# Optimization experiments

Measured on AMD Instinct MI355X. Metric: run time of the kernel, lower is better.

## Reference

```python
import jax, jax.numpy as jnp
import numpy as np

D = 128      # embedding dim
T = 8        # message passing rounds (config.training.T)
NV = 4000    # n_vars
NL = 2 * NV  # n_literals
NC = 16000   # n_clauses


def setup_inputs() -> dict:
    key = jax.random.key(0)
    ks = jax.random.split(key, 12)
    s = np.float32(1.0 / np.sqrt(D))
    return {
        "L_state": jax.random.normal(ks[0], (1, NL, D), jnp.float32),
        "C_state": jax.random.normal(ks[1], (1, NC, D), jnp.float32),
        "hidden_L": jnp.zeros((1, NL, D), jnp.float32),
        "hidden_C": jnp.zeros((1, NC, D), jnp.float32),
        # 0/1 literal-clause incidence, ~40 clauses per literal
        "M": (jax.random.uniform(ks[2], (NL, NC)) < 0.0025).astype(jnp.float32),
        "n_vars": NV,
        "W_lc": jax.random.normal(ks[3], (D, D), jnp.float32) * s,
        "b_lc": jnp.zeros((D,), jnp.float32),
        "W_cl": jax.random.normal(ks[4], (D, D), jnp.float32) * s,
        "b_cl": jnp.zeros((D,), jnp.float32),
        "Wih_C": jax.random.normal(ks[5], (4 * D, D), jnp.float32) * s,
        "Whh_C": jax.random.normal(ks[6], (4 * D, D), jnp.float32) * s,
        "bih_C": jnp.zeros((4 * D,), jnp.float32),
        "bhh_C": jnp.zeros((4 * D,), jnp.float32),
        "Wih_L": jax.random.normal(ks[7], (4 * D, 2 * D), jnp.float32) * s,
        "Whh_L": jax.random.normal(ks[8], (4 * D, D), jnp.float32) * s,
        "bih_L": jnp.zeros((4 * D,), jnp.float32),
        "bhh_L": jnp.zeros((4 * D,), jnp.float32),
    }


def lstm_cell(x, h, c, Wih, Whh, bih, bhh):
    # torch nn.LSTM gate order: i, f, g, o
    gates = x @ Wih.T + bih + h @ Whh.T + bhh
    i, f, g, o = jnp.split(gates, 4, axis=-1)
    c_new = jax.nn.sigmoid(f) * c + jax.nn.sigmoid(i) * jnp.tanh(g)
    h_new = jax.nn.sigmoid(o) * jnp.tanh(c_new)
    return h_new, c_new


def reference(L_state, C_state, hidden_L, hidden_C, M, n_vars,
              W_lc, b_lc, W_cl, b_cl,
              Wih_C, Whh_C, bih_C, bhh_C,
              Wih_L, Whh_L, bih_L, bhh_L):
    # Replicates torch flip() as written: slices dim 0 (size 1), so this is
    # effectively identity for n_vars >= 1 (first slice is empty, second is x).
    def flip(x):
        return jnp.concatenate([x[n_vars:2 * n_vars], x[0:n_vars]], axis=0)

    def step(carry, _):
        L, hL, hC = carry
        LC_pre = L @ W_lc.T + b_lc                        # (1, NL, D)
        LC_msgs = jnp.einsum('lc,sld->scd', M, LC_pre)    # M^T @ pre: (1, NC, D)
        Cs, hC = lstm_cell(LC_msgs, hC, hC, Wih_C, Whh_C, bih_C, bhh_C)
        CL_pre = Cs @ W_cl.T + b_cl                       # (1, NC, D)
        CL_msgs = jnp.einsum('lc,scd->sld', M, CL_pre)    # M @ pre: (1, NL, D)
        inp = jnp.concatenate([CL_msgs, flip(L)], axis=2) # (1, NL, 2D)
        L, hL = lstm_cell(inp, hL, hL, Wih_L, Whh_L, bih_L, bhh_L)
        return (L, hL, hC), None

    (L_final, _, _), _ = jax.lax.scan(step, (L_state, hidden_L, hidden_C), None, length=T)
    return L_final
```

## Files before the change

kernel.cpp:

```cpp
#include <hip/hip_runtime.h>

#define DD   128
#define NL   8000
#define NC   16000
#define TSTEPS 8
#define NBF  2
#define ROWW 96
#define COLW 64

#define OS   33
#define SPLITS8 (32 * OS)
#define SPLIT   (SPLITS8 * 8)
#define LSTR 17
#define LSPL (48 * LSTR * 8)
#define L2S  33
#define L2SPL (48 * L2S * 8)

typedef __attribute__((ext_vector_type(8))) short  short8;
typedef __attribute__((ext_vector_type(8))) _Float16 half8;
typedef __attribute__((ext_vector_type(4))) float  f32x4;

__device__ __forceinline__ float frcp(float x) { return __builtin_amdgcn_rcpf(x); }
__device__ __forceinline__ float sigm(float x) { return frcp(1.f + __expf(-x)); }
__device__ __forceinline__ float tanh_(float x) {
  float e = __expf(2.f * x);
  return 1.f - 2.f * frcp(e + 1.f);
}
__device__ __forceinline__ void add4(float4& a, const float4 b) {
  a.x += b.x; a.y += b.y; a.z += b.z; a.w += b.w;
}
__device__ __forceinline__ unsigned short bfround(float v) {
  unsigned u = __float_as_uint(v);
  return (unsigned short)((u + 0x7FFF + ((u >> 16) & 1)) >> 16);
}
__device__ __forceinline__ float bf2f(unsigned short b) {
  return __uint_as_float(((unsigned)b) << 16);
}
__device__ __forceinline__ void splitf16(float v, unsigned short& h, unsigned short& l) {
  _Float16 hh = (_Float16)v;
  float r = v - (float)hh;
  _Float16 ll = (_Float16)r;
  h = __builtin_bit_cast(unsigned short, hh);
  l = __builtin_bit_cast(unsigned short, ll);
}
__device__ __forceinline__ int4 packi4(const unsigned short* p) {
  return make_int4(p[0] | ((int)p[1] << 16), p[2] | ((int)p[3] << 16),
                   p[4] | ((int)p[5] << 16), p[6] | ((int)p[7] << 16));
}

__device__ __forceinline__ void store_oct3(unsigned short* A, int oct, int m,
                                           float4 a, float4 b) {
  float f[8] = {a.x, a.y, a.z, a.w, b.x, b.y, b.z, b.w};
  unsigned short h[8], md[8], lo[8];
  #pragma unroll
  for (int j = 0; j < 8; ++j) {
    h[j] = bfround(f[j]);
    float r1 = f[j] - bf2f(h[j]);
    md[j] = bfround(r1);
    float r2 = r1 - bf2f(md[j]);
    lo[j] = bfround(r2);
  }
  int base = (oct * OS + m) * 8;
  *(int4*)(A + base)             = packi4(h);
  *(int4*)(A + SPLIT + base)     = packi4(md);
  *(int4*)(A + 2 * SPLIT + base) = packi4(lo);
}

__device__ __forceinline__ void store_oct2g(unsigned short* A, int strideS8, int plane,
                                            int oct, int m, float4 a, float4 b) {
  float f[8] = {a.x, a.y, a.z, a.w, b.x, b.y, b.z, b.w};
  unsigned short h[8], lo[8];
  #pragma unroll
  for (int j = 0; j < 8; ++j) splitf16(f[j], h[j], lo[j]);
  int base = (oct * strideS8 + m) * 8;
  *(int4*)(A + base)         = packi4(h);
  *(int4*)(A + plane + base) = packi4(lo);
}

__device__ __forceinline__ void store_half3L(unsigned short* A, int oct, int half, int m,
                                             float4 a) {
  float f[4] = {a.x, a.y, a.z, a.w};
  unsigned short h[4], md[4], lo[4];
  #pragma unroll
  for (int j = 0; j < 4; ++j) {
    h[j] = bfround(f[j]);
    float r1 = f[j] - bf2f(h[j]);
    md[j] = bfround(r1);
    float r2 = r1 - bf2f(md[j]);
    lo[j] = bfround(r2);
  }
  int base = (oct * LSTR + m) * 8 + half * 4;
  *(int2*)(A + base)            = make_int2(h[0]  | ((int)h[1]  << 16), h[2]  | ((int)h[3]  << 16));
  *(int2*)(A + LSPL + base)     = make_int2(md[0] | ((int)md[1] << 16), md[2] | ((int)md[3] << 16));
  *(int2*)(A + 2 * LSPL + base) = make_int2(lo[0] | ((int)lo[1] << 16), lo[2] | ((int)lo[3] << 16));
}

#define MFMA6(ACC, AH, AM, AL, BH, BM, BL)                                   \
  ACC = __builtin_amdgcn_mfma_f32_16x16x32_bf16(AH, BH, ACC, 0, 0, 0);       \
  ACC = __builtin_amdgcn_mfma_f32_16x16x32_bf16(AH, BM, ACC, 0, 0, 0);       \
  ACC = __builtin_amdgcn_mfma_f32_16x16x32_bf16(AM, BH, ACC, 0, 0, 0);       \
  ACC = __builtin_amdgcn_mfma_f32_16x16x32_bf16(AH, BL, ACC, 0, 0, 0);       \
  ACC = __builtin_amdgcn_mfma_f32_16x16x32_bf16(AL, BH, ACC, 0, 0, 0);       \
  ACC = __builtin_amdgcn_mfma_f32_16x16x32_bf16(AM, BM, ACC, 0, 0, 0);

#define MFMA4(ACC, AH, AL, BH, BL)                                           \
  ACC = __builtin_amdgcn_mfma_f32_16x16x32_f16(AH, BH, ACC, 0, 0, 0);        \
  ACC = __builtin_amdgcn_mfma_f32_16x16x32_f16(AH, BL, ACC, 0, 0, 0);        \
  ACC = __builtin_amdgcn_mfma_f32_16x16x32_f16(AL, BH, ACC, 0, 0, 0);        \
  ACC = __builtin_amdgcn_mfma_f32_16x16x32_f16(AL, BL, ACC, 0, 0, 0);


__global__ __launch_bounds__(256) void init_states(
    float4* __restrict__ Lbuf, const float4* __restrict__ L0,
    float4* __restrict__ hL, const float4* __restrict__ hL0,
    float4* __restrict__ hC, const float4* __restrict__ hC0) {
  int i = blockIdx.x * 256 + threadIdx.x, stride = gridDim.x * 256;
  for (int j = i; j < NL * DD / 4; j += stride) { Lbuf[j] = L0[j]; hL[j] = hL0[j]; }
  for (int j = i; j < NC * DD / 4; j += stride) hC[j] = hC0[j];
}

__global__ __launch_bounds__(256) void scan_M(const float4* __restrict__ M4,
                                              int* __restrict__ csr, int* __restrict__ csc,
                                              int* __restrict__ rcnt, int* __restrict__ ccnt) {
  const int total = (NL * NC) / 4;
  int stride = gridDim.x * blockDim.x;
  for (int i = blockIdx.x * blockDim.x + threadIdx.x; i < total; i += stride) {
    float4 v = M4[i];
    if (v.x == 0.f && v.y == 0.f && v.z == 0.f && v.w == 0.f) continue;
    int base = i * 4;
    int l = base / NC;
    int c0 = base - l * NC;
    float vv[4] = {v.x, v.y, v.z, v.w};
    #pragma unroll
    for (int e = 0; e < 4; ++e) {
      if (vv[e] != 0.f) {
        int c = c0 + e;
        int rp = atomicAdd(&rcnt[l], 1);
        if (rp < ROWW) csr[l * ROWW + rp] = c;
        int cp = atomicAdd(&ccnt[c], 1);
        if (cp < COLW) csc[c * COLW + cp] = l;
      }
    }
  }
}

__device__ __forceinline__ void split_store_bf3(float w, int idx, unsigned short* hi,
                                                unsigned short* md, unsigned short* lo) {
  unsigned short h = bfround(w);
  float r1 = w - bf2f(h);
  unsigned short m = bfround(r1);
  float r2 = r1 - bf2f(m);
  hi[idx] = h; md[idx] = m; lo[idx] = bfround(r2);
}

__global__ __launch_bounds__(256) void build_packC(
    const float* __restrict__ WihC, const float* __restrict__ Wlc, const float* __restrict__ WhhC,
    unsigned short* __restrict__ pkhi, unsigned short* __restrict__ pkmd, unsigned short* __restrict__ pklo,
    unsigned short* __restrict__ qkhi, unsigned short* __restrict__ qklo) {
  int i = blockIdx.x * 256 + threadIdx.x;
  int k = i >> 9, n = i & 511;
  float w;
  if (k < 128) {
    float s = 0.f;
    for (int d = 0; d < 128; ++d) s += WihC[n * 128 + d] * Wlc[d * 128 + k];
    w = s;
  } else {
    w = WhhC[n * 128 + (k - 128)];
  }
  int idx = ((k >> 3) * 512 + n) * 8 + (k & 7);
  split_store_bf3(w, idx, pkhi, pkmd, pklo);
  splitf16(w, qkhi[idx], qklo[idx]);
}

__global__ __launch_bounds__(256) void build_packL(
    const float* __restrict__ WihL, const float* __restrict__ Wcl, const float* __restrict__ WhhL,
    unsigned short* __restrict__ pkhi, unsigned short* __restrict__ pkmd, unsigned short* __restrict__ pklo,
    unsigned short* __restrict__ qkhi, unsigned short* __restrict__ qklo) {
  int i = blockIdx.x * 256 + threadIdx.x;
  int k = i >> 9, n = i & 511;
  float w;
  if (k < 128) {
    float s = 0.f;
    for (int d = 0; d < 128; ++d) s += WihL[n * 256 + d] * Wcl[d * 128 + k];
    w = s;
  } else if (k < 256) {
    w = WihL[n * 256 + k];
  } else {
    w = WhhL[n * 128 + (k - 256)];
  }
  int idx = ((k >> 3) * 512 + n) * 8 + (k & 7);
  split_store_bf3(w, idx, pkhi, pkmd, pklo);
  splitf16(w, qkhi[idx], qklo[idx]);
}

__global__ __launch_bounds__(256) void build_bias(
    const float* __restrict__ bihC, const float* __restrict__ bhhC,
    const float* __restrict__ WihC, const float* __restrict__ blc,
    const float* __restrict__ bihL, const float* __restrict__ bhhL,
    const float* __restrict__ WihL, const float* __restrict__ bcl,
    float* __restrict__ bsumC, float* __restrict__ bvecC,
    float* __restrict__ bsumL, float* __restrict__ bvecL) {
  int i = blockIdx.x * 256 + threadIdx.x;
  if (i < 512) {
    bsumC[i] = bihC[i] + bhhC[i];
    float s = 0.f;
    for (int d = 0; d < 128; ++d) s += WihC[i * 128 + d] * blc[d];
    bvecC[i] = s;
  } else if (i < 1024) {
    int n = i - 512;
    bsumL[n] = bihL[n] + bhhL[n];
    float s = 0.f;
    for (int d = 0; d < 128; ++d) s += WihL[n * 256 + d] * bcl[d];
    bvecL[n] = s;
  }
}

__device__ __forceinline__ void clause_epilogue(
    const f32x4 acc[2][4], const float* bsum, const float* bvec, const int* ccnt,
    float* hC, float* Cs, int rowBase, int quad, int cw) {
  float bs_[4], bv_[4];
  #pragma unroll
  for (int g = 0; g < 4; ++g) { bs_[g] = bsum[g * 128 + cw]; bv_[g] = bvec[g * 128 + cw]; }
  #pragma unroll
  for (int mt = 0; mt < 2; ++mt) {
    #pragma unroll
    for (int reg = 0; reg < 4; ++reg) {
      int row = rowBase + mt * 16 + quad * 4 + reg;
      float deg = (float)ccnt[row];
      float co = hC[(size_t)row * DD + cw];
      float iv = acc[mt][0][reg] + bs_[0] + deg * bv_[0];
      float fv = acc[mt][1][reg] + bs_[1] + deg * bv_[1];
      float gv = acc[mt][2][reg] + bs_[2] + deg * bv_[2];
      float ov = acc[mt][3][reg] + bs_[3] + deg * bv_[3];
      float cn = sigm(fv) * co + sigm(iv) * tanh_(gv);
      hC[(size_t)row * DD + cw] = cn;
      Cs[(size_t)row * DD + cw] = sigm(ov) * tanh_(cn);
    }
  }
}

__device__ __forceinline__ void literal_epilogue2(
    const f32x4 acc[2][4], const float* bsum, const float* bvec, const int* rcnt,
    float* hL, float* Lbuf, int rowBase, int quad, int cw) {
  float bs_[4], bv_[4];
  #pragma unroll
  for (int g = 0; g < 4; ++g) { bs_[g] = bsum[g * 128 + cw]; bv_[g] = bvec[g * 128 + cw]; }
  #pragma unroll
  for (int mt = 0; mt < 2; ++mt) {
    #pragma unroll
    for (int reg = 0; reg < 4; ++reg) {
      int row = rowBase + mt * 16 + quad * 4 + reg;
      float deg = (float)rcnt[row];
      float co = hL[(size_t)row * DD + cw];
      float iv = acc[mt][0][reg] + bs_[0] + deg * bv_[0];
      float fv = acc[mt][1][reg] + bs_[1] + deg * bv_[1];
      float gv = acc[mt][2][reg] + bs_[2] + deg * bv_[2];
      float ov = acc[mt][3][reg] + bs_[3] + deg * bv_[3];
      float cn = sigm(fv) * co + sigm(iv) * tanh_(gv);
      hL[(size_t)row * DD + cw] = cn;
      Lbuf[(size_t)row * DD + cw] = sigm(ov) * tanh_(cn);
    }
  }
}


template <int NOCT, bool STAGE_H>
__global__ __launch_bounds__(512, 4) void clause_bf3(
    const float* __restrict__ Lbuf, const int* __restrict__ csc, const int* __restrict__ ccnt,
    const unsigned short* __restrict__ pkhi, const unsigned short* __restrict__ pkmd,
    const unsigned short* __restrict__ pklo,
    const float* __restrict__ bsum, const float* __restrict__ bvec,
    float* __restrict__ hC, float* __restrict__ Cs) {
  __shared__ unsigned short A[3 * SPLIT];
  __shared__ int IDX[32 * COLW];
  const int t = threadIdx.x;
  const int rowBase = blockIdx.x * 32;

  ((int4*)IDX)[t] = ((const int4*)(csc + rowBase * COLW))[t];
  __syncthreads();

  {
    const int r = t >> 4, sub = t & 15;
    const int c = rowBase + r;
    int cnt = ccnt[c]; if (cnt > COLW) cnt = COLW;
    const int* lst = IDX + r * COLW;
    float4 a0 = make_float4(0, 0, 0, 0), a1 = a0;
    int j = 0;
    for (; j + 8 <= cnt; j += 8) {
      float4 p0[8], p1[8];
      #pragma unroll
      for (int u = 0; u < 8; ++u) {
        const float4* s4 = (const float4*)(Lbuf + (size_t)lst[j + u] * DD) + sub * 2;
        p0[u] = s4[0]; p1[u] = s4[1];
      }
      #pragma unroll
      for (int u = 0; u < 8; ++u) { add4(a0, p0[u]); add4(a1, p1[u]); }
    }
    for (; j < cnt; ++j) {
      const float4* s4 = (const float4*)(Lbuf + (size_t)lst[j] * DD) + sub * 2;
      add4(a0, s4[0]); add4(a1, s4[1]);
    }
    store_oct3(A, sub, r, a0, a1);
    if constexpr (STAGE_H) {
      const float4* h4 = (const float4*)(hC + (size_t)c * DD) + sub * 2;
      store_oct3(A, 16 + sub, r, h4[0], h4[1]);
    }
  }
  __syncthreads();

  const int w = t >> 6, l = t & 63;
  const int quad = l >> 4, lane16 = l & 15;
  const int cw = w * 16 + lane16;
  f32x4 acc[2][4];
  #pragma unroll
  for (int mt = 0; mt < 2; ++mt)
    #pragma unroll
    for (int g = 0; g < 4; ++g) acc[mt][g] = (f32x4){0.f, 0.f, 0.f, 0.f};

  const short8* As = (const short8*)A;
  const short8* Bh = (const short8*)pkhi;
  const short8* Bm = (const short8*)pkmd;
  const short8* Bl = (const short8*)pklo;

  __builtin_amdgcn_s_setprio(1);
  #pragma unroll
  for (int s = 0; s < NOCT / 4; ++s) {
    int ao = (s * 4 + quad) * OS + lane16;
    short8 a0h = As[ao],                a1h = As[ao + 16];
    short8 a0m = As[SPLITS8 + ao],      a1m = As[SPLITS8 + ao + 16];
    short8 a0l = As[2 * SPLITS8 + ao],  a1l = As[2 * SPLITS8 + ao + 16];
    int bo = (s * 4 + quad) * 512 + cw;
    #pragma unroll
    for (int g = 0; g < 4; ++g) {
      short8 bh = Bh[bo + g * 128];
      short8 bm = Bm[bo + g * 128];
      short8 bl = Bl[bo + g * 128];
      MFMA6(acc[0][g], a0h, a0m, a0l, bh, bm, bl);
      MFMA6(acc[1][g], a1h, a1m, a1l, bh, bm, bl);
    }
  }
  __builtin_amdgcn_s_setprio(0);
  clause_epilogue(acc, bsum, bvec, ccnt, hC, Cs, rowBase, quad, cw);
}

template <int NOCT, bool STAGE_H>
__global__ __launch_bounds__(512, 4) void literal_bf3(
    const float* __restrict__ Cs, const int* __restrict__ csr, const int* __restrict__ rcnt,
    const unsigned short* __restrict__ pkhi, const unsigned short* __restrict__ pkmd,
    const unsigned short* __restrict__ pklo,
    const float* __restrict__ bsum, const float* __restrict__ bvec,
    float* __restrict__ hL, float* __restrict__ Lbuf) {
  __shared__ unsigned short A[3 * LSPL];
  __shared__ int IDX[16 * ROWW];
  const int t = threadIdx.x;
  const int rowBase = blockIdx.x * 16;

  if (t < 384) ((int4*)IDX)[t] = ((const int4*)(csr + rowBase * ROWW))[t];
  __syncthreads();

  {
    const int r = t >> 5, cg2 = t & 31;
    const int lr = rowBase + r;
    int cnt = rcnt[lr]; if (cnt > ROWW) cnt = ROWW;
    const int* lst = IDX + r * ROWW;
    float4 a0 = make_float4(0, 0, 0, 0);
    int j = 0;
    for (; j + 8 <= cnt; j += 8) {
      float4 p[8];
      #pragma unroll
      for (int u = 0; u < 8; ++u)
        p[u] = ((const float4*)(Cs + (size_t)lst[j + u] * DD))[cg2];
      #pragma unroll
      for (int u = 0; u < 8; ++u) add4(a0, p[u]);
    }
    for (; j < cnt; ++j)
      add4(a0, ((const float4*)(Cs + (size_t)lst[j] * DD))[cg2]);
    store_half3L(A, cg2 >> 1, cg2 & 1, r, a0);
    store_half3L(A, 16 + (cg2 >> 1), cg2 & 1, r,
                 ((const float4*)(Lbuf + (size_t)lr * DD))[cg2]);
    if constexpr (STAGE_H)
      store_half3L(A, 32 + (cg2 >> 1), cg2 & 1, r,
                   ((const float4*)(hL + (size_t)lr * DD))[cg2]);
  }
  __syncthreads();

  const int w = t >> 6, l = t & 63;
  const int quad = l >> 4, lane16 = l & 15;
  const int cw = w * 16 + lane16;
  f32x4 acc[4];
  #pragma unroll
  for (int g = 0; g < 4; ++g) acc[g] = (f32x4){0.f, 0.f, 0.f, 0.f};

  const short8* As = (const short8*)A;
  const short8* Bh = (const short8*)pkhi;
  const short8* Bm = (const short8*)pkmd;
  const short8* Bl = (const short8*)pklo;

  __builtin_amdgcn_s_setprio(1);
  #pragma unroll
  for (int s = 0; s < NOCT / 4; ++s) {
    int ao = (s * 4 + quad) * LSTR + lane16;
    short8 ah = As[ao];
    short8 am = As[LSPL / 8 + ao];
    short8 al = As[2 * (LSPL / 8) + ao];
    int bo = (s * 4 + quad) * 512 + cw;
    #pragma unroll
    for (int g = 0; g < 4; ++g) {
      short8 bh = Bh[bo + g * 128];
      short8 bm = Bm[bo + g * 128];
      short8 bl = Bl[bo + g * 128];
      MFMA6(acc[g], ah, am, al, bh, bm, bl);
    }
  }
  __builtin_amdgcn_s_setprio(0);

  float bs_[4], bv_[4];
  #pragma unroll
  for (int g = 0; g < 4; ++g) { bs_[g] = bsum[g * 128 + cw]; bv_[g] = bvec[g * 128 + cw]; }
  #pragma unroll
  for (int reg = 0; reg < 4; ++reg) {
    int row = rowBase + quad * 4 + reg;
    float deg = (float)rcnt[row];
    float co = hL[(size_t)row * DD + cw];
    float iv = acc[0][reg] + bs_[0] + deg * bv_[0];
    float fv = acc[1][reg] + bs_[1] + deg * bv_[1];
    float gv = acc[2][reg] + bs_[2] + deg * bv_[2];
    float ov = acc[3][reg] + bs_[3] + deg * bv_[3];
    float cn = sigm(fv) * co + sigm(iv) * tanh_(gv);
    hL[(size_t)row * DD + cw] = cn;
    Lbuf[(size_t)row * DD + cw] = sigm(ov) * tanh_(cn);
  }
}


__global__ __launch_bounds__(512, 4) void clause_f2(
    const float* __restrict__ Lbuf, const int* __restrict__ csc, const int* __restrict__ ccnt,
    const unsigned short* __restrict__ qkhi, const unsigned short* __restrict__ qklo,
    const float* __restrict__ bsum, const float* __restrict__ bvec,
    float* __restrict__ hC, float* __restrict__ Cs) {
  __shared__ unsigned short A[2 * SPLIT];
  __shared__ int IDX[32 * COLW];
  const int t = threadIdx.x;
  const int rowBase = blockIdx.x * 32;

  ((int4*)IDX)[t] = ((const int4*)(csc + rowBase * COLW))[t];
  __syncthreads();

  {
    const int r = t >> 4, sub = t & 15;
    const int c = rowBase + r;
    int cnt = ccnt[c]; if (cnt > COLW) cnt = COLW;
    const int* lst = IDX + r * COLW;
    float4 a0 = make_float4(0, 0, 0, 0), a1 = a0;
    int j = 0;
    for (; j + 8 <= cnt; j += 8) {
      float4 p0[8], p1[8];
      #pragma unroll
      for (int u = 0; u < 8; ++u) {
        const float4* s4 = (const float4*)(Lbuf + (size_t)lst[j + u] * DD) + sub * 2;
        p0[u] = s4[0]; p1[u] = s4[1];
      }
      #pragma unroll
      for (int u = 0; u < 8; ++u) { add4(a0, p0[u]); add4(a1, p1[u]); }
    }
    for (; j < cnt; ++j) {
      const float4* s4 = (const float4*)(Lbuf + (size_t)lst[j] * DD) + sub * 2;
      add4(a0, s4[0]); add4(a1, s4[1]);
    }
    store_oct2g(A, OS, SPLIT, sub, r, a0, a1);
    const float4* h4 = (const float4*)(hC + (size_t)c * DD) + sub * 2;
    store_oct2g(A, OS, SPLIT, 16 + sub, r, h4[0], h4[1]);
  }
  __syncthreads();

  const int w = t >> 6, l = t & 63;
  const int quad = l >> 4, lane16 = l & 15;
  const int cw = w * 16 + lane16;
  f32x4 acc[2][4];
  #pragma unroll
  for (int mt = 0; mt < 2; ++mt)
    #pragma unroll
    for (int g = 0; g < 4; ++g) acc[mt][g] = (f32x4){0.f, 0.f, 0.f, 0.f};

  const half8* As = (const half8*)A;
  const half8* Bh = (const half8*)qkhi;
  const half8* Bl = (const half8*)qklo;

  __builtin_amdgcn_s_setprio(1);
  #pragma unroll
  for (int s = 0; s < 8; ++s) {
    int ao = (s * 4 + quad) * OS + lane16;
    half8 a0h = As[ao],           a1h = As[ao + 16];
    half8 a0l = As[SPLITS8 + ao], a1l = As[SPLITS8 + ao + 16];
    int bo = (s * 4 + quad) * 512 + cw;
    #pragma unroll
    for (int g = 0; g < 4; ++g) {
      half8 bh = Bh[bo + g * 128];
      half8 bl = Bl[bo + g * 128];
      MFMA4(acc[0][g], a0h, a0l, bh, bl);
      MFMA4(acc[1][g], a1h, a1l, bh, bl);
    }
  }
  __builtin_amdgcn_s_setprio(0);
  clause_epilogue(acc, bsum, bvec, ccnt, hC, Cs, rowBase, quad, cw);
}

__global__ __launch_bounds__(512, 4) void literal_f2(
    const float* __restrict__ Cs, const int* __restrict__ csr, const int* __restrict__ rcnt,
    const unsigned short* __restrict__ qkhi, const unsigned short* __restrict__ qklo,
    const float* __restrict__ bsum, const float* __restrict__ bvec,
    float* __restrict__ hL, float* __restrict__ Lbuf) {
  __shared__ unsigned short A[2 * L2SPL];
  __shared__ int IDX[32 * ROWW];
  const int t = threadIdx.x;
  const int rowBase = blockIdx.x * 32;

  ((int4*)IDX)[t] = ((const int4*)(csr + rowBase * ROWW))[t];
  if (t < 256) ((int4*)IDX)[t + 512] = ((const int4*)(csr + rowBase * ROWW))[t + 512];
  __syncthreads();

  {
    const int r = t >> 4, sub = t & 15;
    const int lr = rowBase + r;
    int cnt = rcnt[lr]; if (cnt > ROWW) cnt = ROWW;
    const int* lst = IDX + r * ROWW;
    float4 a0 = make_float4(0, 0, 0, 0), a1 = a0;
    int j = 0;
    for (; j + 8 <= cnt; j += 8) {
      float4 p0[8], p1[8];
      #pragma unroll
      for (int u = 0; u < 8; ++u) {
        const float4* s4 = (const float4*)(Cs + (size_t)lst[j + u] * DD) + sub * 2;
        p0[u] = s4[0]; p1[u] = s4[1];
      }
      #pragma unroll
      for (int u = 0; u < 8; ++u) { add4(a0, p0[u]); add4(a1, p1[u]); }
    }
    for (; j < cnt; ++j) {
      const float4* s4 = (const float4*)(Cs + (size_t)lst[j] * DD) + sub * 2;
      add4(a0, s4[0]); add4(a1, s4[1]);
    }
    store_oct2g(A, L2S, L2SPL, sub, r, a0, a1);
    const float4* l4 = (const float4*)(Lbuf + (size_t)lr * DD) + sub * 2;
    store_oct2g(A, L2S, L2SPL, 16 + sub, r, l4[0], l4[1]);
    const float4* h4 = (const float4*)(hL + (size_t)lr * DD) + sub * 2;
    store_oct2g(A, L2S, L2SPL, 32 + sub, r, h4[0], h4[1]);
  }
  __syncthreads();

  const int w = t >> 6, l = t & 63;
  const int quad = l >> 4, lane16 = l & 15;
  const int cw = w * 16 + lane16;
  f32x4 acc[2][4];
  #pragma unroll
  for (int mt = 0; mt < 2; ++mt)
    #pragma unroll
    for (int g = 0; g < 4; ++g) acc[mt][g] = (f32x4){0.f, 0.f, 0.f, 0.f};

  const half8* As = (const half8*)A;
  const half8* Bh = (const half8*)qkhi;
  const half8* Bl = (const half8*)qklo;

  __builtin_amdgcn_s_setprio(1);
  #pragma unroll
  for (int s = 0; s < 12; ++s) {
    int ao = (s * 4 + quad) * L2S + lane16;
    half8 a0h = As[ao],             a1h = As[ao + 16];
    half8 a0l = As[L2SPL / 8 + ao], a1l = As[L2SPL / 8 + ao + 16];
    int bo = (s * 4 + quad) * 512 + cw;
    #pragma unroll
    for (int g = 0; g < 4; ++g) {
      half8 bh = Bh[bo + g * 128];
      half8 bl = Bl[bo + g * 128];
      MFMA4(acc[0][g], a0h, a0l, bh, bl);
      MFMA4(acc[1][g], a1h, a1l, bh, bl);
    }
  }
  __builtin_amdgcn_s_setprio(0);
  literal_epilogue2(acc, bsum, bvec, rcnt, hL, Lbuf, rowBase, quad, cw);
}


extern "C" void kernel_launch(void* const* d_in, const int* in_sizes, int n_in,
                              void* d_out, int out_size, void* d_ws, size_t ws_size,
                              hipStream_t stream) {
  const float* L0   = (const float*)d_in[0];
  const float* hL0  = (const float*)d_in[2];
  const float* hC0  = (const float*)d_in[3];
  const float* M    = (const float*)d_in[4];
  const float* Wlc  = (const float*)d_in[6];
  const float* blc  = (const float*)d_in[7];
  const float* Wcl  = (const float*)d_in[8];
  const float* bcl  = (const float*)d_in[9];
  const float* WihC = (const float*)d_in[10];
  const float* WhhC = (const float*)d_in[11];
  const float* bihC = (const float*)d_in[12];
  const float* bhhC = (const float*)d_in[13];
  const float* WihL = (const float*)d_in[14];
  const float* WhhL = (const float*)d_in[15];
  const float* bihL = (const float*)d_in[16];
  const float* bhhL = (const float*)d_in[17];

  float* ws    = (float*)d_ws;
  float* hL    = ws;
  float* hC    = hL + NL * DD;
  float* Cs    = hC + NC * DD;
  float* bsumC = Cs + NC * DD;
  float* bvecC = bsumC + 512;
  float* bsumL = bvecC + 512;
  float* bvecL = bsumL + 512;
  unsigned short* pkChi = (unsigned short*)(bvecL + 512);
  unsigned short* pkCmd = pkChi + 256 * 512;
  unsigned short* pkClo = pkCmd + 256 * 512;
  unsigned short* pkLhi = pkClo + 256 * 512;
  unsigned short* pkLmd = pkLhi + 384 * 512;
  unsigned short* pkLlo = pkLmd + 384 * 512;
  unsigned short* qkChi = pkLlo + 384 * 512;
  unsigned short* qkClo = qkChi + 256 * 512;
  unsigned short* qkLhi = qkClo + 256 * 512;
  unsigned short* qkLlo = qkLhi + 384 * 512;
  int* csr  = (int*)(qkLlo + 384 * 512);
  int* csc  = csr + NL * ROWW;
  int* rcnt = csc + NC * COLW;
  int* ccnt = rcnt + NL;
  float* Lbuf = (float*)d_out;

  hipMemsetAsync(rcnt, 0, (NL + NC) * sizeof(int), stream);

  init_states<<<1024, 256, 0, stream>>>((float4*)Lbuf, (const float4*)L0,
                                        (float4*)hL, (const float4*)hL0,
                                        (float4*)hC, (const float4*)hC0);

  scan_M<<<4096, 256, 0, stream>>>((const float4*)M, csr, csc, rcnt, ccnt);

  build_packC<<<(256 * 512) / 256, 256, 0, stream>>>(WihC, Wlc, WhhC,
                                                     pkChi, pkCmd, pkClo, qkChi, qkClo);
  build_packL<<<(384 * 512) / 256, 256, 0, stream>>>(WihL, Wcl, WhhL,
                                                     pkLhi, pkLmd, pkLlo, qkLhi, qkLlo);
  build_bias<<<4, 256, 0, stream>>>(bihC, bhhC, WihC, blc, bihL, bhhL, WihL, bcl,
                                    bsumC, bvecC, bsumL, bvecL);

  clause_bf3<16, false><<<NC / 32, 512, 0, stream>>>(Lbuf, csc, ccnt, pkChi, pkCmd, pkClo,
                                                     bsumC, bvecC, hC, Cs);
  literal_bf3<32, false><<<NL / 16, 512, 0, stream>>>(Cs, csr, rcnt, pkLhi, pkLmd, pkLlo,
                                                      bsumL, bvecL, hL, Lbuf);
  for (int t = 1; t < NBF; ++t) {
    clause_bf3<32, true><<<NC / 32, 512, 0, stream>>>(Lbuf, csc, ccnt, pkChi, pkCmd, pkClo,
                                                      bsumC, bvecC, hC, Cs);
    literal_bf3<48, true><<<NL / 16, 512, 0, stream>>>(Cs, csr, rcnt, pkLhi, pkLmd, pkLlo,
                                                       bsumL, bvecL, hL, Lbuf);
  }
  for (int t = NBF; t < TSTEPS; ++t) {
    clause_f2<<<NC / 32, 512, 0, stream>>>(Lbuf, csc, ccnt, qkChi, qkClo,
                                           bsumC, bvecC, hC, Cs);
    literal_f2<<<NL / 32, 512, 0, stream>>>(Cs, csr, rcnt, qkLhi, qkLlo,
                                            bsumL, bvecL, hL, Lbuf);
  }
}
```

Baseline: 1.280 ms.

## Fuse all stages into one persistent cooperative kernel with grid syncs

Replaces the roughly twenty separate launches (memset, init, CSR/CSC scan, weight packing, bias, and the per-step clause and literal kernels) with a single cooperative kernel of 256 blocks. The stages are separated by grid-wide syncs, and each block loops over tiles using a union of the shared-memory layouts. The aim is to remove per-launch overhead and the inter-kernel gaps. The cost is that 256 blocks of 512 threads may give lower occupancy than the earlier larger grids, tiles split unevenly across blocks (500 clause tiles over 256 blocks), and the shared union is sized by its largest member for every stage.

```diff
diff --git a/kernel.cpp b/kernel.cpp
--- a/kernel.cpp
+++ b/kernel.cpp
@@ -1,4 +1,7 @@
 #include <hip/hip_runtime.h>
+#include <hip/hip_cooperative_groups.h>
+
+namespace cg = cooperative_groups;
 
 #define DD   128
 #define NL   8000
@@ -7,6 +10,7 @@
 #define NBF  2
 #define ROWW 96
 #define COLW 64
+#define GRID 256
 
 #define OS   33
 #define SPLITS8 (32 * OS)
@@ -95,6 +99,15 @@
   *(int2*)(A + 2 * LSPL + base) = make_int2(lo[0] | ((int)lo[1] << 16), lo[2] | ((int)lo[3] << 16));
 }
 
+__device__ __forceinline__ void split_store_bf3(float w, int idx, unsigned short* hi,
+                                                unsigned short* md, unsigned short* lo) {
+  unsigned short h = bfround(w);
+  float r1 = w - bf2f(h);
+  unsigned short m = bfround(r1);
+  float r2 = r1 - bf2f(m);
+  hi[idx] = h; md[idx] = m; lo[idx] = bfround(r2);
+}
+
 #define MFMA6(ACC, AH, AM, AL, BH, BM, BL)                                   \
   ACC = __builtin_amdgcn_mfma_f32_16x16x32_bf16(AH, BH, ACC, 0, 0, 0);       \
   ACC = __builtin_amdgcn_mfma_f32_16x16x32_bf16(AH, BM, ACC, 0, 0, 0);       \
@@ -109,111 +122,12 @@
   ACC = __builtin_amdgcn_mfma_f32_16x16x32_f16(AL, BH, ACC, 0, 0, 0);        \
   ACC = __builtin_amdgcn_mfma_f32_16x16x32_f16(AL, BL, ACC, 0, 0, 0);
 
-
-__global__ __launch_bounds__(256) void init_states(
-    float4* __restrict__ Lbuf, const float4* __restrict__ L0,
-    float4* __restrict__ hL, const float4* __restrict__ hL0,
-    float4* __restrict__ hC, const float4* __restrict__ hC0) {
-  int i = blockIdx.x * 256 + threadIdx.x, stride = gridDim.x * 256;
-  for (int j = i; j < NL * DD / 4; j += stride) { Lbuf[j] = L0[j]; hL[j] = hL0[j]; }
-  for (int j = i; j < NC * DD / 4; j += stride) hC[j] = hC0[j];
-}
-
-__global__ __launch_bounds__(256) void scan_M(const float4* __restrict__ M4,
-                                              int* __restrict__ csr, int* __restrict__ csc,
-                                              int* __restrict__ rcnt, int* __restrict__ ccnt) {
-  const int total = (NL * NC) / 4;
-  int stride = gridDim.x * blockDim.x;
-  for (int i = blockIdx.x * blockDim.x + threadIdx.x; i < total; i += stride) {
-    float4 v = M4[i];
-    if (v.x == 0.f && v.y == 0.f && v.z == 0.f && v.w == 0.f) continue;
-    int base = i * 4;
-    int l = base / NC;
-    int c0 = base - l * NC;
-    float vv[4] = {v.x, v.y, v.z, v.w};
-    #pragma unroll
-    for (int e = 0; e < 4; ++e) {
-      if (vv[e] != 0.f) {
-        int c = c0 + e;
-        int rp = atomicAdd(&rcnt[l], 1);
-        if (rp < ROWW) csr[l * ROWW + rp] = c;
-        int cp = atomicAdd(&ccnt[c], 1);
-        if (cp < COLW) csc[c * COLW + cp] = l;
-      }
-    }
-  }
-}
-
-__device__ __forceinline__ void split_store_bf3(float w, int idx, unsigned short* hi,
-                                                unsigned short* md, unsigned short* lo) {
-  unsigned short h = bfround(w);
-  float r1 = w - bf2f(h);
-  unsigned short m = bfround(r1);
-  float r2 = r1 - bf2f(m);
-  hi[idx] = h; md[idx] = m; lo[idx] = bfround(r2);
-}
-
-__global__ __launch_bounds__(256) void build_packC(
-    const float* __restrict__ WihC, const float* __restrict__ Wlc, const float* __restrict__ WhhC,
-    unsigned short* __restrict__ pkhi, unsigned short* __restrict__ pkmd, unsigned short* __restrict__ pklo,
-    unsigned short* __restrict__ qkhi, unsigned short* __restrict__ qklo) {
-  int i = blockIdx.x * 256 + threadIdx.x;
-  int k = i >> 9, n = i & 511;
-  float w;
-  if (k < 128) {
-    float s = 0.f;
-    for (int d = 0; d < 128; ++d) s += WihC[n * 128 + d] * Wlc[d * 128 + k];
-    w = s;
-  } else {
-    w = WhhC[n * 128 + (k - 128)];
-  }
-  int idx = ((k >> 3) * 512 + n) * 8 + (k & 7);
-  split_store_bf3(w, idx, pkhi, pkmd, pklo);
-  splitf16(w, qkhi[idx], qklo[idx]);
-}
-
-__global__ __launch_bounds__(256) void build_packL(
-    const float* __restrict__ WihL, const float* __restrict__ Wcl, const float* __restrict__ WhhL,
-    unsigned short* __restrict__ pkhi, unsigned short* __restrict__ pkmd, unsigned short* __restrict__ pklo,
-    unsigned short* __restrict__ qkhi, unsigned short* __restrict__ qklo) {
-  int i = blockIdx.x * 256 + threadIdx.x;
-  int k = i >> 9, n = i & 511;
-  float w;
-  if (k < 128) {
-    float s = 0.f;
-    for (int d = 0; d < 128; ++d) s += WihL[n * 256 + d] * Wcl[d * 128 + k];
-    w = s;
-  } else if (k < 256) {
-    w = WihL[n * 256 + k];
-  } else {
-    w = WhhL[n * 128 + (k - 256)];
-  }
-  int idx = ((k >> 3) * 512 + n) * 8 + (k & 7);
-  split_store_bf3(w, idx, pkhi, pkmd, pklo);
-  splitf16(w, qkhi[idx], qklo[idx]);
-}
-
-__global__ __launch_bounds__(256) void build_bias(
-    const float* __restrict__ bihC, const float* __restrict__ bhhC,
-    const float* __restrict__ WihC, const float* __restrict__ blc,
-    const float* __restrict__ bihL, const float* __restrict__ bhhL,
-    const float* __restrict__ WihL, const float* __restrict__ bcl,
-    float* __restrict__ bsumC, float* __restrict__ bvecC,
-    float* __restrict__ bsumL, float* __restrict__ bvecL) {
-  int i = blockIdx.x * 256 + threadIdx.x;
-  if (i < 512) {
-    bsumC[i] = bihC[i] + bhhC[i];
-    float s = 0.f;
-    for (int d = 0; d < 128; ++d) s += WihC[i * 128 + d] * blc[d];
-    bvecC[i] = s;
-  } else if (i < 1024) {
-    int n = i - 512;
-    bsumL[n] = bihL[n] + bhhL[n];
-    float s = 0.f;
-    for (int d = 0; d < 128; ++d) s += WihL[n * 256 + d] * bcl[d];
-    bvecL[n] = s;
-  }
-}
+union alignas(16) SmemU {
+  struct { unsigned short A[3 * SPLIT];  int IDX[32 * COLW]; } cb3;
+  struct { unsigned short A[3 * LSPL];   int IDX[16 * ROWW]; } lb3;
+  struct { unsigned short A[2 * SPLIT];  int IDX[32 * COLW]; } cf2;
+  struct { unsigned short A[2 * L2SPL];  int IDX[32 * ROWW]; } lf2;
+};
 
 __device__ __forceinline__ void clause_epilogue(
     const f32x4 acc[2][4], const float* bsum, const float* bvec, const int* ccnt,
@@ -265,16 +179,17 @@
 
 
 template <int NOCT, bool STAGE_H>
-__global__ __launch_bounds__(512, 4) void clause_bf3(
+__device__ __forceinline__ void clause_bf3_tile(
+    SmemU& sm, int tile,
     const float* __restrict__ Lbuf, const int* __restrict__ csc, const int* __restrict__ ccnt,
     const unsigned short* __restrict__ pkhi, const unsigned short* __restrict__ pkmd,
     const unsigned short* __restrict__ pklo,
     const float* __restrict__ bsum, const float* __restrict__ bvec,
     float* __restrict__ hC, float* __restrict__ Cs) {
-  __shared__ unsigned short A[3 * SPLIT];
-  __shared__ int IDX[32 * COLW];
+  unsigned short* A = sm.cb3.A;
+  int* IDX = sm.cb3.IDX;
   const int t = threadIdx.x;
-  const int rowBase = blockIdx.x * 32;
+  const int rowBase = tile * 32;
 
   ((int4*)IDX)[t] = ((const int4*)(csc + rowBase * COLW))[t];
   __syncthreads();
@@ -344,16 +259,17 @@
 }
 
 template <int NOCT, bool STAGE_H>
-__global__ __launch_bounds__(512, 4) void literal_bf3(
+__device__ __forceinline__ void literal_bf3_tile(
+    SmemU& sm, int tile,
     const float* __restrict__ Cs, const int* __restrict__ csr, const int* __restrict__ rcnt,
     const unsigned short* __restrict__ pkhi, const unsigned short* __restrict__ pkmd,
     const unsigned short* __restrict__ pklo,
     const float* __restrict__ bsum, const float* __restrict__ bvec,
     float* __restrict__ hL, float* __restrict__ Lbuf) {
-  __shared__ unsigned short A[3 * LSPL];
-  __shared__ int IDX[16 * ROWW];
+  unsigned short* A = sm.lb3.A;
+  int* IDX = sm.lb3.IDX;
   const int t = threadIdx.x;
-  const int rowBase = blockIdx.x * 16;
+  const int rowBase = tile * 16;
 
   if (t < 384) ((int4*)IDX)[t] = ((const int4*)(csr + rowBase * ROWW))[t];
   __syncthreads();
@@ -432,16 +348,16 @@
   }
 }
 
-
-__global__ __launch_bounds__(512, 4) void clause_f2(
+__device__ __forceinline__ void clause_f2_tile(
+    SmemU& sm, int tile,
     const float* __restrict__ Lbuf, const int* __restrict__ csc, const int* __restrict__ ccnt,
     const unsigned short* __restrict__ qkhi, const unsigned short* __restrict__ qklo,
     const float* __restrict__ bsum, const float* __restrict__ bvec,
     float* __restrict__ hC, float* __restrict__ Cs) {
-  __shared__ unsigned short A[2 * SPLIT];
-  __shared__ int IDX[32 * COLW];
+  unsigned short* A = sm.cf2.A;
+  int* IDX = sm.cf2.IDX;
   const int t = threadIdx.x;
-  const int rowBase = blockIdx.x * 32;
+  const int rowBase = tile * 32;
 
   ((int4*)IDX)[t] = ((const int4*)(csc + rowBase * COLW))[t];
   __syncthreads();
@@ -505,15 +421,16 @@
   clause_epilogue(acc, bsum, bvec, ccnt, hC, Cs, rowBase, quad, cw);
 }
 
-__global__ __launch_bounds__(512, 4) void literal_f2(
+__device__ __forceinline__ void literal_f2_tile(
+    SmemU& sm, int tile,
     const float* __restrict__ Cs, const int* __restrict__ csr, const int* __restrict__ rcnt,
     const unsigned short* __restrict__ qkhi, const unsigned short* __restrict__ qklo,
     const float* __restrict__ bsum, const float* __restrict__ bvec,
     float* __restrict__ hL, float* __restrict__ Lbuf) {
-  __shared__ unsigned short A[2 * L2SPL];
-  __shared__ int IDX[32 * ROWW];
+  unsigned short* A = sm.lf2.A;
+  int* IDX = sm.lf2.IDX;
   const int t = threadIdx.x;
-  const int rowBase = blockIdx.x * 32;
+  const int rowBase = tile * 32;
 
   ((int4*)IDX)[t] = ((const int4*)(csr + rowBase * ROWW))[t];
   if (t < 256) ((int4*)IDX)[t + 512] = ((const int4*)(csr + rowBase * ROWW))[t + 512];
@@ -578,6 +495,137 @@
   }
   __builtin_amdgcn_s_setprio(0);
   literal_epilogue2(acc, bsum, bvec, rcnt, hL, Lbuf, rowBase, quad, cw);
+}
+
+
+struct MegaArgs {
+  const float *L0, *hL0, *hC0;
+  const float4 *M4;
+  const float *Wlc, *blc, *Wcl, *bcl;
+  const float *WihC, *WhhC, *bihC, *bhhC;
+  const float *WihL, *WhhL, *bihL, *bhhL;
+  float *hL, *hC, *Cs, *bsumC, *bvecC, *bsumL, *bvecL;
+  unsigned short *pkChi, *pkCmd, *pkClo, *pkLhi, *pkLmd, *pkLlo;
+  unsigned short *qkChi, *qkClo, *qkLhi, *qkLlo;
+  int *csr, *csc, *rcnt, *ccnt;
+  float *Lbuf;
+};
+
+#define GSYNC() do { __threadfence(); grid.sync(); } while (0)
+
+__global__ __launch_bounds__(512, 2) void mega(MegaArgs a) {
+  __shared__ SmemU sm;
+  cg::grid_group grid = cg::this_grid();
+  const int gtid = blockIdx.x * 512 + threadIdx.x;
+  const int gstride = GRID * 512;
+
+  for (int j = gtid; j < NL * DD / 4; j += gstride) {
+    ((float4*)a.Lbuf)[j] = ((const float4*)a.L0)[j];
+    ((float4*)a.hL)[j]   = ((const float4*)a.hL0)[j];
+  }
+  for (int j = gtid; j < NC * DD / 4; j += gstride)
+    ((float4*)a.hC)[j] = ((const float4*)a.hC0)[j];
+  for (int j = gtid; j < NL + NC; j += gstride) a.rcnt[j] = 0;
+  GSYNC();
+
+  {
+    const int total = (NL * NC) / 4;
+    for (int i = gtid; i < total; i += gstride) {
+      float4 v = a.M4[i];
+      if (v.x == 0.f && v.y == 0.f && v.z == 0.f && v.w == 0.f) continue;
+      int base = i * 4;
+      int l = base / NC;
+      int c0 = base - l * NC;
+      float vv[4] = {v.x, v.y, v.z, v.w};
+      #pragma unroll
+      for (int e = 0; e < 4; ++e) {
+        if (vv[e] != 0.f) {
+          int c = c0 + e;
+          int rp = atomicAdd(&a.rcnt[l], 1);
+          if (rp < ROWW) a.csr[l * ROWW + rp] = c;
+          int cp = atomicAdd(&a.ccnt[c], 1);
+          if (cp < COLW) a.csc[c * COLW + cp] = l;
+        }
+      }
+    }
+  }
+  GSYNC();
+
+  for (int i = gtid; i < 256 * 512; i += gstride) {
+    int k = i >> 9, n = i & 511;
+    float w;
+    if (k < 128) {
+      float s = 0.f;
+      for (int d = 0; d < 128; ++d) s += a.WihC[n * 128 + d] * a.Wlc[d * 128 + k];
+      w = s;
+    } else {
+      w = a.WhhC[n * 128 + (k - 128)];
+    }
+    int idx = ((k >> 3) * 512 + n) * 8 + (k & 7);
+    split_store_bf3(w, idx, a.pkChi, a.pkCmd, a.pkClo);
+    splitf16(w, a.qkChi[idx], a.qkClo[idx]);
+  }
+  for (int i = gtid; i < 384 * 512; i += gstride) {
+    int k = i >> 9, n = i & 511;
+    float w;
+    if (k < 128) {
+      float s = 0.f;
+      for (int d = 0; d < 128; ++d) s += a.WihL[n * 256 + d] * a.Wcl[d * 128 + k];
+      w = s;
+    } else if (k < 256) {
+      w = a.WihL[n * 256 + k];
+    } else {
+      w = a.WhhL[n * 128 + (k - 256)];
+    }
+    int idx = ((k >> 3) * 512 + n) * 8 + (k & 7);
+    split_store_bf3(w, idx, a.pkLhi, a.pkLmd, a.pkLlo);
+    splitf16(w, a.qkLhi[idx], a.qkLlo[idx]);
+  }
+  if (gtid < 1024) {
+    int i = gtid;
+    if (i < 512) {
+      a.bsumC[i] = a.bihC[i] + a.bhhC[i];
+      float s = 0.f;
+      for (int d = 0; d < 128; ++d) s += a.WihC[i * 128 + d] * a.blc[d];
+      a.bvecC[i] = s;
+    } else {
+      int n = i - 512;
+      a.bsumL[n] = a.bihL[n] + a.bhhL[n];
+      float s = 0.f;
+      for (int d = 0; d < 128; ++d) s += a.WihL[n * 256 + d] * a.bcl[d];
+      a.bvecL[n] = s;
+    }
+  }
+  GSYNC();
+
+  for (int tile = blockIdx.x; tile < NC / 32; tile += GRID)
+    clause_bf3_tile<16, false>(sm, tile, a.Lbuf, a.csc, a.ccnt,
+                               a.pkChi, a.pkCmd, a.pkClo, a.bsumC, a.bvecC, a.hC, a.Cs);
+  GSYNC();
+  for (int tile = blockIdx.x; tile < NL / 16; tile += GRID)
+    literal_bf3_tile<32, false>(sm, tile, a.Cs, a.csr, a.rcnt,
+                                a.pkLhi, a.pkLmd, a.pkLlo, a.bsumL, a.bvecL, a.hL, a.Lbuf);
+  GSYNC();
+
+  for (int tile = blockIdx.x; tile < NC / 32; tile += GRID)
+    clause_bf3_tile<32, true>(sm, tile, a.Lbuf, a.csc, a.ccnt,
+                              a.pkChi, a.pkCmd, a.pkClo, a.bsumC, a.bvecC, a.hC, a.Cs);
+  GSYNC();
+  for (int tile = blockIdx.x; tile < NL / 16; tile += GRID)
+    literal_bf3_tile<48, true>(sm, tile, a.Cs, a.csr, a.rcnt,
+                               a.pkLhi, a.pkLmd, a.pkLlo, a.bsumL, a.bvecL, a.hL, a.Lbuf);
+  GSYNC();
+
+  for (int st = NBF; st < TSTEPS; ++st) {
+    for (int tile = blockIdx.x; tile < NC / 32; tile += GRID)
+      clause_f2_tile(sm, tile, a.Lbuf, a.csc, a.ccnt,
+                     a.qkChi, a.qkClo, a.bsumC, a.bvecC, a.hC, a.Cs);
+    GSYNC();
+    for (int tile = blockIdx.x; tile < NL / 32; tile += GRID)
+      literal_f2_tile(sm, tile, a.Cs, a.csr, a.rcnt,
+                      a.qkLhi, a.qkLlo, a.bsumL, a.bvecL, a.hL, a.Lbuf);
+    if (st != TSTEPS - 1) GSYNC();
+  }
 }
 
 
@@ -625,35 +673,19 @@
   int* ccnt = rcnt + NL;
   float* Lbuf = (float*)d_out;
 
-  hipMemsetAsync(rcnt, 0, (NL + NC) * sizeof(int), stream);
-
-  init_states<<<1024, 256, 0, stream>>>((float4*)Lbuf, (const float4*)L0,
-                                        (float4*)hL, (const float4*)hL0,
-                                        (float4*)hC, (const float4*)hC0);
-
-  scan_M<<<4096, 256, 0, stream>>>((const float4*)M, csr, csc, rcnt, ccnt);
-
-  build_packC<<<(256 * 512) / 256, 256, 0, stream>>>(WihC, Wlc, WhhC,
-                                                     pkChi, pkCmd, pkClo, qkChi, qkClo);
-  build_packL<<<(384 * 512) / 256, 256, 0, stream>>>(WihL, Wcl, WhhL,
-                                                     pkLhi, pkLmd, pkLlo, qkLhi, qkLlo);
-  build_bias<<<4, 256, 0, stream>>>(bihC, bhhC, WihC, blc, bihL, bhhL, WihL, bcl,
-                                    bsumC, bvecC, bsumL, bvecL);
-
-  clause_bf3<16, false><<<NC / 32, 512, 0, stream>>>(Lbuf, csc, ccnt, pkChi, pkCmd, pkClo,
-                                                     bsumC, bvecC, hC, Cs);
-  literal_bf3<32, false><<<NL / 16, 512, 0, stream>>>(Cs, csr, rcnt, pkLhi, pkLmd, pkLlo,
-                                                      bsumL, bvecL, hL, Lbuf);
-  for (int t = 1; t < NBF; ++t) {
-    clause_bf3<32, true><<<NC / 32, 512, 0, stream>>>(Lbuf, csc, ccnt, pkChi, pkCmd, pkClo,
-                                                      bsumC, bvecC, hC, Cs);
-    literal_bf3<48, true><<<NL / 16, 512, 0, stream>>>(Cs, csr, rcnt, pkLhi, pkLmd, pkLlo,
-                                                       bsumL, bvecL, hL, Lbuf);
-  }
-  for (int t = NBF; t < TSTEPS; ++t) {
-    clause_f2<<<NC / 32, 512, 0, stream>>>(Lbuf, csc, ccnt, qkChi, qkClo,
-                                           bsumC, bvecC, hC, Cs);
-    literal_f2<<<NL / 32, 512, 0, stream>>>(Cs, csr, rcnt, qkLhi, qkLlo,
-                                            bsumL, bvecL, hL, Lbuf);
-  }
-}
+  MegaArgs args;
+  args.L0 = L0; args.hL0 = hL0; args.hC0 = hC0; args.M4 = (const float4*)M;
+  args.Wlc = Wlc; args.blc = blc; args.Wcl = Wcl; args.bcl = bcl;
+  args.WihC = WihC; args.WhhC = WhhC; args.bihC = bihC; args.bhhC = bhhC;
+  args.WihL = WihL; args.WhhL = WhhL; args.bihL = bihL; args.bhhL = bhhL;
+  args.hL = hL; args.hC = hC; args.Cs = Cs;
+  args.bsumC = bsumC; args.bvecC = bvecC; args.bsumL = bsumL; args.bvecL = bvecL;
+  args.pkChi = pkChi; args.pkCmd = pkCmd; args.pkClo = pkClo;
+  args.pkLhi = pkLhi; args.pkLmd = pkLmd; args.pkLlo = pkLlo;
+  args.qkChi = qkChi; args.qkClo = qkClo; args.qkLhi = qkLhi; args.qkLlo = qkLlo;
+  args.csr = csr; args.csc = csc; args.rcnt = rcnt; args.ccnt = ccnt;
+  args.Lbuf = Lbuf;
+
+  void* kp[] = {(void*)&args};
+  hipLaunchCooperativeKernel((const void*)mega, dim3(GRID), dim3(512), kp, 0, stream);
+}
```

Measured after the change: 3.155 ms. +146.5%, slower.
